# Kernel tuning notes

Hardware: AMD Instinct MI355X
Metric: run time of the kernel (lower is better)

## Reference

```python
import jax, jax.numpy as jnp
import numpy as np

B, T, G, P = 16, 256, 1024, 16          # batch, num_tf, num_genes, peaks per gene
N, GO_DIM = 4096, 6                      # num_gos, go_dim (hard-coded in module)
HEADS, OUT_CH = 2, 4                     # selfGATConv(go_dim, 4, heads=2)
E = 65536                                # num edges
NUM_OUT = 32


def lrelu(x, slope):
    return jnp.where(x >= 0, x, slope * x)


def setup_inputs() -> dict:
    ks = jax.random.split(jax.random.key(0), 12)
    x = jax.random.normal(ks[0], (B, T, G * P), dtype=jnp.float32)
    edge_index = jax.random.randint(ks[1], (2, E), 0, N, dtype=jnp.int64)
    # per-gene subNet: Linear(num_peak*num_tf, 1) -> weight [G, T, P], bias [G]
    W_sub = jax.random.normal(ks[2], (G, T, P), dtype=jnp.float32) * 0.02
    b_sub = jax.random.normal(ks[3], (G,), dtype=jnp.float32) * 0.02
    fc1_weight = jax.random.normal(ks[4], (N * GO_DIM, G), dtype=jnp.float32) * 0.02
    mask = (jax.random.uniform(ks[5], (N, G)) < 0.05).astype(jnp.float32)
    mask_rep = jnp.repeat(mask, GO_DIM, axis=0)  # [N*GO_DIM, G]
    fc1_bias = jax.random.normal(ks[6], (N * GO_DIM,), dtype=jnp.float32) * 0.02
    gat_weight = jax.random.normal(ks[7], (GO_DIM, HEADS * OUT_CH), dtype=jnp.float32) * 0.3
    gat_att = jax.random.normal(ks[8], (1, 1, HEADS, 2 * OUT_CH), dtype=jnp.float32) * 0.3
    gat_bias = jax.random.normal(ks[9], (OUT_CH,), dtype=jnp.float32) * 0.02
    out_weight = jax.random.normal(ks[10], (NUM_OUT, N * OUT_CH), dtype=jnp.float32) * 0.02
    out_bias = jax.random.normal(ks[11], (NUM_OUT,), dtype=jnp.float32) * 0.02
    return {"x": x, "edge_index": edge_index, "W_sub": W_sub, "b_sub": b_sub,
            "fc1_weight": fc1_weight, "mask_rep": mask_rep, "fc1_bias": fc1_bias,
            "gat_weight": gat_weight, "gat_att": gat_att, "gat_bias": gat_bias,
            "out_weight": out_weight, "out_bias": out_bias}


def reference(x, edge_index, W_sub, b_sub, fc1_weight, mask_rep, fc1_bias,
              gat_weight, gat_att, gat_bias, out_weight, out_bias):
    # --- per-gene subnets (uniform num_peaks -> block-diag as one einsum) ---
    xg = x.reshape(B, T, G, P)                        # contiguous cut blocks
    x_cat = jnp.einsum('btgp,gtp->bg', xg, W_sub) + b_sub   # [B, G]
    x_cat = lrelu(x_cat, 0.01)                        # nn.LeakyReLU default
    # --- masked dense linear -> GO-term hidden layer ---
    h = x_cat @ (fc1_weight * mask_rep).T + fc1_bias  # [B, N*GO_DIM]
    h = lrelu(h, 0.01)
    h = h.reshape(B, GO_DIM, N).transpose(2, 0, 1)    # [N, B, GO_DIM]
    # --- selfGATConv: gather -> leaky_relu score -> seg-softmax -> scatter-mean ---
    hn = (h @ gat_weight).reshape(N, B, HEADS, OUT_CH)  # [N, B, H, C]
    src, dst = edge_index[0], edge_index[1]
    x_j = hn[src]                                     # [E, B, H, C]
    x_i = hn[dst]
    att = gat_att[0, 0]                               # [H, 2C]
    alpha = (jnp.einsum('ebhc,hc->ebh', x_i, att[:, :OUT_CH]) +
             jnp.einsum('ebhc,hc->ebh', x_j, att[:, OUT_CH:]))
    alpha = lrelu(alpha, 0.2)                         # negative_slope=0.2
    amax = jax.ops.segment_max(alpha, dst, num_segments=N)
    alpha = jnp.exp(alpha - amax[dst])
    denom = jax.ops.segment_sum(alpha, dst, num_segments=N)
    alpha = alpha / denom[dst]                        # per-destination softmax
    msg = x_j * alpha[..., None]                      # [E, B, H, C]
    summed = jax.ops.segment_sum(msg, dst, num_segments=N)
    cnt = jax.ops.segment_sum(jnp.ones((E,), jnp.float32), dst, num_segments=N)
    aggr = summed / jnp.maximum(cnt, 1.0)[:, None, None, None]  # aggr='mean'
    aggr = aggr.mean(axis=2) + gat_bias               # concat=False: mean heads -> [N, B, C]
    # --- readout ---
    o = aggr.transpose(1, 2, 0).reshape(B, OUT_CH * N)
    o = lrelu(o, 0.01)                                # dropout is identity in eval
    return o @ out_weight.T + out_bias                # [B, NUM_OUT]
```

## Files before the change

kernel.cpp:

```cpp
#include <hip/hip_runtime.h>
#include <math.h>

#define KB 16
#define KT 256
#define KG 1024
#define KP 16
#define KN 4096
#define KGO 6
#define KH 2
#define KC 4
#define KE 65536
#define KOUT 32

__device__ __forceinline__ float lrelu(float x, float s) { return x >= 0.f ? x : s * x; }

__global__ __launch_bounds__(256) void k0_detect(const int* __restrict__ e32,
                                                 int* __restrict__ flag) {
    __shared__ int nz;
    if (threadIdx.x == 0) nz = 0;
    __syncthreads();
    int any = 0;
#pragma unroll
    for (int k = 0; k < 4; ++k) {
        int idx = (threadIdx.x * 4 + k) * 2 + 1;
        any |= (e32[idx] != 0) ? 1 : 0;
    }
    if (any) atomicOr(&nz, 1);
    __syncthreads();
    if (threadIdx.x == 0) flag[0] = (nz == 0) ? 1 : 0;
}

__global__ __launch_bounds__(256) void k1_subnet(const float* __restrict__ x,
                                                 const float* __restrict__ Wsub,
                                                 const float* __restrict__ bsub,
                                                 float* __restrict__ xcat) {
    int wave = blockIdx.x * 4 + (threadIdx.x >> 6);
    int lane = threadIdx.x & 63;
    int b = wave >> 10;
    int g = wave & 1023;
    const float* xb = x + (size_t)b * (KT * KG * KP) + (size_t)g * KP;
    const float* wg = Wsub + (size_t)g * (KT * KP);
    float4 acc = make_float4(0.f, 0.f, 0.f, 0.f);
#pragma unroll 4
    for (int i = 0; i < 16; ++i) {
        int q = lane + 64 * i;
        int t = q >> 2;
        int p4 = (q & 3) * 4;
        float4 xv = *(const float4*)(xb + (size_t)t * (KG * KP) + p4);
        float4 wv = *(const float4*)(wg + q * 4);
        acc.x += xv.x * wv.x; acc.y += xv.y * wv.y;
        acc.z += xv.z * wv.z; acc.w += xv.w * wv.w;
    }
    float s = acc.x + acc.y + acc.z + acc.w;
#pragma unroll
    for (int off = 32; off > 0; off >>= 1) s += __shfl_down(s, off, 64);
    if (lane == 0) xcat[b * KG + g] = lrelu(s + bsub[g], 0.01f);
}

__global__ __launch_bounds__(256) void k2_fc1(const float* __restrict__ w,
                                              const float* __restrict__ mask,
                                              const float* __restrict__ bias,
                                              const float* __restrict__ xcat,
                                              float* __restrict__ ht) {
    int wid = threadIdx.x >> 6;
    int lane = threadIdx.x & 63;
    int b0 = wid * 4;
    float4 xcr[4][4];
#pragma unroll
    for (int bb = 0; bb < 4; ++bb)
#pragma unroll
        for (int i = 0; i < 4; ++i)
            xcr[bb][i] = *(const float4*)(xcat + (b0 + bb) * KG + i * 256 + lane * 4);

    for (int r = 0; r < 16; ++r) {
        int j = blockIdx.x * 16 + r;
        const float* wr = w + (size_t)j * KG;
        const float* mr = mask + (size_t)j * KG;
        float acc0 = 0.f, acc1 = 0.f, acc2 = 0.f, acc3 = 0.f;
#pragma unroll
        for (int i = 0; i < 4; ++i) {
            float4 wv = *(const float4*)(wr + i * 256 + lane * 4);
            float4 mv = *(const float4*)(mr + i * 256 + lane * 4);
            float px = wv.x * mv.x, py = wv.y * mv.y, pz = wv.z * mv.z, pw = wv.w * mv.w;
            acc0 += px * xcr[0][i].x + py * xcr[0][i].y + pz * xcr[0][i].z + pw * xcr[0][i].w;
            acc1 += px * xcr[1][i].x + py * xcr[1][i].y + pz * xcr[1][i].z + pw * xcr[1][i].w;
            acc2 += px * xcr[2][i].x + py * xcr[2][i].y + pz * xcr[2][i].z + pw * xcr[2][i].w;
            acc3 += px * xcr[3][i].x + py * xcr[3][i].y + pz * xcr[3][i].z + pw * xcr[3][i].w;
        }
#pragma unroll
        for (int m = 1; m < 64; m <<= 1) {
            acc0 += __shfl_xor(acc0, m, 64);
            acc1 += __shfl_xor(acc1, m, 64);
            acc2 += __shfl_xor(acc2, m, 64);
            acc3 += __shfl_xor(acc3, m, 64);
        }
        if (lane == 0) {
            float bj = bias[j];
            int d = j >> 12;
            int n = j & 4095;
            float* hp = ht + ((size_t)n * KB) * KGO + d;
            hp[(b0 + 0) * KGO] = lrelu(acc0 + bj, 0.01f);
            hp[(b0 + 1) * KGO] = lrelu(acc1 + bj, 0.01f);
            hp[(b0 + 2) * KGO] = lrelu(acc2 + bj, 0.01f);
            hp[(b0 + 3) * KGO] = lrelu(acc3 + bj, 0.01f);
        }
    }
}

__global__ __launch_bounds__(256) void k3_gatw(const float* __restrict__ ht,
                                               const float* __restrict__ gw,
                                               const float* __restrict__ att,
                                               float* __restrict__ hn,
                                               float* __restrict__ si,
                                               float* __restrict__ sj) {
    __shared__ float cgw[48];
    __shared__ float catt[16];
    int t = threadIdx.x;
    if (t < 48) cgw[t] = gw[t];
    else if (t < 64) catt[t - 48] = att[t - 48];
    __syncthreads();
    int idx = blockIdx.x * 256 + t;
    float h6[6];
#pragma unroll
    for (int d = 0; d < 6; ++d) h6[d] = ht[(size_t)idx * KGO + d];
    float o[8];
#pragma unroll
    for (int hc = 0; hc < 8; ++hc) {
        float v = 0.f;
#pragma unroll
        for (int d = 0; d < 6; ++d) v += h6[d] * cgw[d * 8 + hc];
        o[hc] = v;
        hn[(size_t)idx * 8 + hc] = v;
    }
#pragma unroll
    for (int hh = 0; hh < 2; ++hh) {
        float vi = 0.f, vj = 0.f;
#pragma unroll
        for (int c = 0; c < 4; ++c) {
            vi += o[hh * 4 + c] * catt[hh * 8 + c];
            vj += o[hh * 4 + c] * catt[hh * 8 + 4 + c];
        }
        si[idx * 2 + hh] = vi;
        sj[idx * 2 + hh] = vj;
    }
}

__global__ __launch_bounds__(256) void k4a_hist(const int* __restrict__ e32,
                                                const int* __restrict__ flag,
                                                int* __restrict__ cnt) {
    int e = blockIdx.x * 256 + threadIdx.x;
    int mode = flag[0];
    int d = mode ? e32[2 * (KE + e)] : e32[KE + e];
    atomicAdd(&cnt[d], 1);
}

__global__ __launch_bounds__(1024) void k4b_scan(const int* __restrict__ cnt,
                                                 int* __restrict__ off,
                                                 int* __restrict__ cur) {
    __shared__ int buf[2][1024];
    int t = threadIdx.x;
    int c0 = cnt[t * 4 + 0], c1 = cnt[t * 4 + 1], c2 = cnt[t * 4 + 2], c3 = cnt[t * 4 + 3];
    int s = c0 + c1 + c2 + c3;
    buf[0][t] = s;
    __syncthreads();
    int pb = 0;
    for (int d = 1; d < 1024; d <<= 1) {
        int v = buf[pb][t];
        if (t >= d) v += buf[pb][t - d];
        buf[1 - pb][t] = v;
        pb = 1 - pb;
        __syncthreads();
    }
    int incl = buf[pb][t];
    int base = incl - s;
    int o0 = base, o1 = base + c0, o2 = base + c0 + c1, o3 = base + c0 + c1 + c2;
    off[t * 4 + 0] = o0; off[t * 4 + 1] = o1; off[t * 4 + 2] = o2; off[t * 4 + 3] = o3;
    cur[t * 4 + 0] = o0; cur[t * 4 + 1] = o1; cur[t * 4 + 2] = o2; cur[t * 4 + 3] = o3;
    if (t == 1023) off[KN] = incl;
}

__global__ __launch_bounds__(256) void k4c_scatter(const int* __restrict__ e32,
                                                   const int* __restrict__ flag,
                                                   int* __restrict__ cur,
                                                   int* __restrict__ csr) {
    int e = blockIdx.x * 256 + threadIdx.x;
    int mode = flag[0];
    int d = mode ? e32[2 * (KE + e)] : e32[KE + e];
    int s = mode ? e32[2 * e] : e32[e];
    int p = atomicAdd(&cur[d], 1);
    csr[p] = s;
}

__global__ __launch_bounds__(256) void k5_gat(const int* __restrict__ offs,
                                              const int* __restrict__ csr,
                                              const float* __restrict__ si,
                                              const float* __restrict__ sj,
                                              const float* __restrict__ hn,
                                              const float* __restrict__ gbias,
                                              float* __restrict__ aggr) {
    int n = blockIdx.x;
    int t = threadIdx.x;
    int p = t >> 3;
    int s = t & 7;
    int b = p >> 1, h = p & 1;
    int off = offs[n];
    int deg = offs[n + 1] - off;
    __shared__ float red[32][4];
    float l = 0.f, a0 = 0.f, a1 = 0.f, a2 = 0.f, a3 = 0.f;
    if (deg > 0) {
        float sib = si[(n * KB + b) * 2 + h];
        float m = -1e30f;
        for (int i = s; i < deg; i += 8) {
            int sv = csr[off + i];
            float a = sib + sj[(sv * KB + b) * 2 + h];
            a = a >= 0.f ? a : 0.2f * a;
            m = fmaxf(m, a);
        }
        m = fmaxf(m, __shfl_xor(m, 1, 64));
        m = fmaxf(m, __shfl_xor(m, 2, 64));
        m = fmaxf(m, __shfl_xor(m, 4, 64));
        for (int i = s; i < deg; i += 8) {
            int sv = csr[off + i];
            float a = sib + sj[(sv * KB + b) * 2 + h];
            a = a >= 0.f ? a : 0.2f * a;
            float wgt = expf(a - m);
            l += wgt;
            float4 hv = *(const float4*)(hn + ((size_t)(sv * KB + b)) * 8 + h * 4);
            a0 += wgt * hv.x; a1 += wgt * hv.y; a2 += wgt * hv.z; a3 += wgt * hv.w;
        }
#pragma unroll
        for (int d = 1; d <= 4; d <<= 1) {
            l  += __shfl_xor(l,  d, 64);
            a0 += __shfl_xor(a0, d, 64);
            a1 += __shfl_xor(a1, d, 64);
            a2 += __shfl_xor(a2, d, 64);
            a3 += __shfl_xor(a3, d, 64);
        }
    }
    if (s == 0) {
        float inv = (deg > 0) ? 1.f / l : 0.f;
        red[p][0] = a0 * inv; red[p][1] = a1 * inv;
        red[p][2] = a2 * inv; red[p][3] = a3 * inv;
    }
    __syncthreads();
    if (t < 64) {
        int bb = t >> 2, c = t & 3;
        float v = gbias[c];
        if (deg > 0)
            v += 0.5f * (red[bb * 2 + 0][c] + red[bb * 2 + 1][c]) / (float)deg;
        aggr[bb * (KC * KN) + c * KN + n] = v;
    }
}

__global__ __launch_bounds__(256) void k6_out(const float* __restrict__ aggr,
                                              const float* __restrict__ ow,
                                              const float* __restrict__ obias,
                                              float* __restrict__ out) {
    int b = blockIdx.x >> 5;
    int k = blockIdx.x & 31;
    int t = threadIdx.x;
    const float* ar = aggr + (size_t)b * (KC * KN);
    const float* wr = ow + (size_t)k * (KC * KN);
    float sum = 0.f;
#pragma unroll 4
    for (int i = 0; i < 16; ++i) {
        int j = (i * 256 + t) * 4;
        float4 av = *(const float4*)(ar + j);
        float4 wv = *(const float4*)(wr + j);
        av.x = lrelu(av.x, 0.01f); av.y = lrelu(av.y, 0.01f);
        av.z = lrelu(av.z, 0.01f); av.w = lrelu(av.w, 0.01f);
        sum += av.x * wv.x + av.y * wv.y + av.z * wv.z + av.w * wv.w;
    }
#pragma unroll
    for (int d = 32; d > 0; d >>= 1) sum += __shfl_down(sum, d, 64);
    __shared__ float wsum[4];
    if ((t & 63) == 0) wsum[t >> 6] = sum;
    __syncthreads();
    if (t == 0) out[b * KOUT + k] = wsum[0] + wsum[1] + wsum[2] + wsum[3] + obias[k];
}

extern "C" void kernel_launch(void* const* d_in, const int* in_sizes, int n_in,
                              void* d_out, int out_size, void* d_ws, size_t ws_size,
                              hipStream_t stream) {
    const float* x     = (const float*)d_in[0];
    const int*   e32   = (const int*)d_in[1];
    const float* Wsub  = (const float*)d_in[2];
    const float* bsub  = (const float*)d_in[3];
    const float* fc1w  = (const float*)d_in[4];
    const float* maskr = (const float*)d_in[5];
    const float* fc1b  = (const float*)d_in[6];
    const float* gatw  = (const float*)d_in[7];
    const float* gata  = (const float*)d_in[8];
    const float* gatb  = (const float*)d_in[9];
    const float* outw  = (const float*)d_in[10];
    const float* outb  = (const float*)d_in[11];
    float* out = (float*)d_out;

    float* ws   = (float*)d_ws;
    float* xcat = ws;
    float* ht   = xcat + KB * KG;
    float* hn   = ht + (size_t)KN * KB * KGO;
    float* si   = hn + (size_t)KN * KB * KH * KC;
    float* sj   = si + (size_t)KN * KB * KH;
    float* aggr = sj + (size_t)KN * KB * KH;
    int* icnt  = (int*)(aggr + (size_t)KB * KC * KN);
    int* ioff  = icnt + KN;
    int* icur  = ioff + (KN + 16);
    int* icsr  = icur + KN;
    int* iflag = icsr + KE;

    k0_detect<<<1, 256, 0, stream>>>(e32, iflag);
    k1_subnet<<<(KB * KG) / 4, 256, 0, stream>>>(x, Wsub, bsub, xcat);
    k2_fc1<<<(KN * KGO) / 16, 256, 0, stream>>>(fc1w, maskr, fc1b, xcat, ht);
    k3_gatw<<<(KN * KB) / 256, 256, 0, stream>>>(ht, gatw, gata, hn, si, sj);
    hipMemsetAsync(icnt, 0, KN * sizeof(int), stream);
    k4a_hist<<<KE / 256, 256, 0, stream>>>(e32, iflag, icnt);
    k4b_scan<<<1, 1024, 0, stream>>>(icnt, ioff, icur);
    k4c_scatter<<<KE / 256, 256, 0, stream>>>(e32, iflag, icur, icsr);
    k5_gat<<<KN, 256, 0, stream>>>(ioff, icsr, si, sj, hn, gatb, aggr);
    k6_out<<<KB * KOUT, 256, 0, stream>>>(aggr, outw, outb, out);
}
```

Before: 572.1 us.

## Restructure subnet kernel so each block reads contiguous gene rows per timestep

The per-gene subnet reduction changes from one wave per (batch, gene) doing strided 64-byte reads to 1024-thread blocks covering 64 consecutive genes for one batch. Each timestep row is now read as a contiguous 4 KB segment, and the T dimension is split across four sub-groups that are reduced through shared memory. This aims to improve coalescing of the dominant 268 MB read of x. In exchange, only 256 blocks are launched and there is a shared-memory sync.

```diff
diff --git a/kernel.cpp b/kernel.cpp
--- a/kernel.cpp
+++ b/kernel.cpp
@@ -30,31 +30,40 @@
     if (threadIdx.x == 0) flag[0] = (nz == 0) ? 1 : 0;
 }
 
-__global__ __launch_bounds__(256) void k1_subnet(const float* __restrict__ x,
-                                                 const float* __restrict__ Wsub,
-                                                 const float* __restrict__ bsub,
-                                                 float* __restrict__ xcat) {
-    int wave = blockIdx.x * 4 + (threadIdx.x >> 6);
-    int lane = threadIdx.x & 63;
-    int b = wave >> 10;
-    int g = wave & 1023;
-    const float* xb = x + (size_t)b * (KT * KG * KP) + (size_t)g * KP;
-    const float* wg = Wsub + (size_t)g * (KT * KP);
+__global__ __launch_bounds__(1024) void k1_subnet(const float* __restrict__ x,
+                                                  const float* __restrict__ Wsub,
+                                                  const float* __restrict__ bsub,
+                                                  float* __restrict__ xcat) {
+    int tid = threadIdx.x;
+    int sub = tid >> 8;
+    int u   = tid & 255;
+    int gc  = blockIdx.x >> 4;
+    int b   = blockIdx.x & 15;
+    int g0  = gc * 64;
+    int g   = g0 + (u >> 2);
+    int p4  = (u & 3) * 4;
+    const float* xb = x + (size_t)b * (KT * KG * KP) + (size_t)g0 * KP + u * 4;
+    const float* wg = Wsub + (size_t)g * (KT * KP) + p4;
     float4 acc = make_float4(0.f, 0.f, 0.f, 0.f);
+    int t0 = sub * 64;
 #pragma unroll 4
-    for (int i = 0; i < 16; ++i) {
-        int q = lane + 64 * i;
-        int t = q >> 2;
-        int p4 = (q & 3) * 4;
-        float4 xv = *(const float4*)(xb + (size_t)t * (KG * KP) + p4);
-        float4 wv = *(const float4*)(wg + q * 4);
+    for (int i = 0; i < 64; ++i) {
+        int t = t0 + i;
+        float4 xv = *(const float4*)(xb + (size_t)t * (KG * KP));
+        float4 wv = *(const float4*)(wg + (size_t)t * KP);
         acc.x += xv.x * wv.x; acc.y += xv.y * wv.y;
         acc.z += xv.z * wv.z; acc.w += xv.w * wv.w;
     }
     float s = acc.x + acc.y + acc.z + acc.w;
-#pragma unroll
-    for (int off = 32; off > 0; off >>= 1) s += __shfl_down(s, off, 64);
-    if (lane == 0) xcat[b * KG + g] = lrelu(s + bsub[g], 0.01f);
+    s += __shfl_xor(s, 1, 64);
+    s += __shfl_xor(s, 2, 64);
+    __shared__ float part[4][64];
+    if ((u & 3) == 0) part[sub][u >> 2] = s;
+    __syncthreads();
+    if (tid < 64) {
+        float v = part[0][tid] + part[1][tid] + part[2][tid] + part[3][tid];
+        xcat[b * KG + g0 + tid] = lrelu(v + bsub[g0 + tid], 0.01f);
+    }
 }
 
 __global__ __launch_bounds__(256) void k2_fc1(const float* __restrict__ w,
@@ -310,7 +319,7 @@
     int* iflag = icsr + KE;
 
     k0_detect<<<1, 256, 0, stream>>>(e32, iflag);
-    k1_subnet<<<(KB * KG) / 4, 256, 0, stream>>>(x, Wsub, bsub, xcat);
+    k1_subnet<<<256, 1024, 0, stream>>>(x, Wsub, bsub, xcat);
     k2_fc1<<<(KN * KGO) / 16, 256, 0, stream>>>(fc1w, maskr, fc1b, xcat, ht);
     k3_gatw<<<(KN * KB) / 256, 256, 0, stream>>>(ht, gatw, gata, hn, si, sj);
     hipMemsetAsync(icnt, 0, KN * sizeof(int), stream);
```

Result: faster. 557.7 us (-2.5%).
